# Kernel optimization log

Hardware: AMD Instinct MI355X
Metric: run time of the kernel (lower is better)

The kernel has to match this reference:

```python
import jax, jax.numpy as jnp
import numpy as np

RHO = 1.0          # ADMM penalty
LAM = 0.1          # lambda_sparse
MAX_ITERS = 20
ZETA = 0.05        # APAS drift threshold / CDS temperature
TAU = 0.1          # chiral stabilizer tolerance
STEP = 0.1         # gradient step size
COHESION = 1.0     # Mohr-Coulomb cohesion
MU = 0.5           # Mohr-Coulomb friction coefficient
DP_K = 10.0        # Drucker-Prager deviatoric-norm radius


def _pas(c):
    # Phase Alignment Invariant: scalar phase-coherence metric in [0,1]
    return jnp.abs(jnp.mean(jnp.cos(c)))


def _chirality(c):
    # odd (sign-sensitive) global moment
    return jnp.mean(c ** 3)


def _mc_proj(c, g):
    # Mohr-Coulomb yield projection: clamp magnitude to cohesion + mu*|grad|
    return jnp.sign(c) * jnp.minimum(jnp.abs(c), COHESION + MU * jnp.abs(g))


def _dp_proj(c):
    # Drucker-Prager: project deviatoric part onto norm ball of radius DP_K (per row)
    m = jnp.mean(c, axis=-1, keepdims=True)
    dev = c - m
    n = jnp.linalg.norm(dev, axis=-1, keepdims=True)
    scale = jnp.minimum(1.0, DP_K / (n + 1e-8))
    return m + dev * scale


def setup_inputs() -> dict:
    key = jax.random.key(0)
    k1, k2, k3 = jax.random.split(key, 3)
    B, D = 1024, 2048
    initial_c = 0.5 * jax.random.normal(k1, (B, D), dtype=jnp.float32)
    W = jax.random.normal(k2, (D, D), dtype=jnp.float32) / np.float32(np.sqrt(D))
    love_w = 1.0 + 0.01 * jax.random.normal(k3, (D,), dtype=jnp.float32)
    love_b = jnp.zeros((D,), dtype=jnp.float32)
    return {"initial_c": initial_c, "W": W, "love_w": love_w, "love_b": love_b}


def _forward(initial_c, W, love_w, love_b):
    c_sym = initial_c
    c0 = initial_c
    z0 = c0
    u0 = jnp.zeros_like(c0)
    prev_pas0 = _pas(c0)
    prev_score0 = -_chirality(c0)  # drift = 0 -> exp(0) = 1

    def step(carry, _):
        c, z, u, prev_pas, prev_score, low, done = carry

        def energy(ci):
            pred = ci @ W  # forward_op_fn
            violation_pressure = 0.5 * jnp.sum((pred - ci) ** 2)
            admm_tension = 0.5 * RHO * jnp.sum((ci - z + u) ** 2)
            return violation_pressure + admm_tension

        g = jax.grad(energy)(c)
        c_yield = _mc_proj(c, g)
        c_next = (c_yield * love_w + love_b) - STEP * g  # LoveVector then step
        z_in = c_next + u
        thr = LAM / RHO
        z_next = jnp.sign(z_in) * jnp.maximum(jnp.abs(z_in) - thr, 0.0)
        u_next = u + (c_next - z_next)

        cur_pas = _pas(c_next)
        drift = jnp.abs(cur_pas - prev_pas)
        violation = drift > ZETA
        low = jnp.where(cur_pas < 0.5, low + 1, 0)
        done = done | (low > 20)
        cur_score = -_chirality(c_next) * jnp.exp(-drift / ZETA)
        stable = (cur_score - prev_score) >= -TAU
        acc = (~violation) & stable & (~done)

        sel = lambda a, b: jnp.where(acc, a, b)
        new = (sel(c_next, c), sel(z_next, z), sel(u_next, u),
               jnp.where(acc, cur_pas, prev_pas),
               jnp.where(acc, cur_score, prev_score), low, done)
        return new, None

    init = (c0, z0, u0, prev_pas0, prev_score0,
            jnp.zeros((), jnp.int32), jnp.zeros((), jnp.bool_))
    (c_phys, z, u, _, _, _, _), _ = jax.lax.scan(step, init, None, length=MAX_ITERS)

    diff = jnp.linalg.norm(c_phys - c_sym)
    chi_cur = _chirality(c_phys)
    chi_orig = _chirality(c_sym)
    status = jnp.where(jnp.sign(chi_cur) != jnp.sign(chi_orig),
                       2,
                       jnp.where(diff > 5.0, 2, jnp.where(diff > 1.0, 1, 0))).astype(jnp.int32)

    delta = c_phys - c_sym
    symbolic_delta = jnp.round(delta * 10.0) / 10.0
    c_compressed = _dp_proj(c_sym + symbolic_delta)
    return c_compressed, status


def reference(initial_c, W, love_w, love_b):
    return _forward(initial_c, W, love_w, love_b)
```

## Files before the change

kernel.cpp:

```cpp
#include <hip/hip_runtime.h>
#include <math.h>

#define D 2048
#define BROWS 1024
#define NEL (D*BROWS)
#define NBLK 1024
#define NTHREADS_TOT (NBLK*256)

#define GM 64
#define GN 64
#define GK 16

__device__ __forceinline__ double blk_reduce(double v, double* sm) {
    const int t = threadIdx.x;
    sm[t] = v;
    __syncthreads();
    for (int s = 128; s > 0; s >>= 1) {
        if (t < s) sm[t] += sm[t + s];
        __syncthreads();
    }
    double r = sm[0];
    __syncthreads();
    return r;
}

__global__ __launch_bounds__(128, 2) void k_gemm(const float* __restrict__ A,
        const float* __restrict__ B, float* __restrict__ P0, float* __restrict__ P1,
        const float* __restrict__ Wadj, int ksz, int mode, const int* __restrict__ frz)
{
    if (frz && *frz) return;
    __shared__ float As[2][GK][GM + 4];
    __shared__ float Bs[2][GK][GN + 4];
    const int t  = threadIdx.x;
    const int tx = t & 7, ty = t >> 3;
    const int row0 = blockIdx.y * GM, col0 = blockIdx.x * GN;
    const int k0 = blockIdx.z * ksz;
    float* __restrict__ out = blockIdx.z ? P1 : P0;

    const int rs = t >> 2, qs = t & 3;
    const float* pA0 = A + (size_t)(row0 + rs) * D + (k0 + qs * 4);
    const float* pA1 = pA0 + (size_t)32 * D;
    const float* pB0 = B + (size_t)(col0 + rs) * D + (k0 + qs * 4);
    const float* pB1 = pB0 + (size_t)32 * D;

    float acc[4][8];
    #pragma unroll
    for (int i = 0; i < 4; ++i)
        #pragma unroll
        for (int j = 0; j < 8; ++j) acc[i][j] = 0.0f;

    const int ntiles = ksz / GK;
    float4 ga0, ga1, gb0, gb1;

#define LOADR { \
    ga0 = *reinterpret_cast<const float4*>(pA0); \
    ga1 = *reinterpret_cast<const float4*>(pA1); \
    gb0 = *reinterpret_cast<const float4*>(pB0); \
    gb1 = *reinterpret_cast<const float4*>(pB1); \
    pA0 += GK; pA1 += GK; pB0 += GK; pB1 += GK; }

#define STAGE(BUF) { \
    As[BUF][qs*4+0][rs] = ga0.x;  As[BUF][qs*4+1][rs] = ga0.y;  \
    As[BUF][qs*4+2][rs] = ga0.z;  As[BUF][qs*4+3][rs] = ga0.w;  \
    As[BUF][qs*4+0][rs+32] = ga1.x; As[BUF][qs*4+1][rs+32] = ga1.y; \
    As[BUF][qs*4+2][rs+32] = ga1.z; As[BUF][qs*4+3][rs+32] = ga1.w; \
    Bs[BUF][qs*4+0][rs] = gb0.x;  Bs[BUF][qs*4+1][rs] = gb0.y;  \
    Bs[BUF][qs*4+2][rs] = gb0.z;  Bs[BUF][qs*4+3][rs] = gb0.w;  \
    Bs[BUF][qs*4+0][rs+32] = gb1.x; Bs[BUF][qs*4+1][rs+32] = gb1.y; \
    Bs[BUF][qs*4+2][rs+32] = gb1.z; Bs[BUF][qs*4+3][rs+32] = gb1.w; }

#define COMPUTE(BUF) { \
    _Pragma("unroll") \
    for (int k = 0; k < GK; ++k) { \
        float a[4], b[8]; \
        *reinterpret_cast<float4*>(&a[0]) = *reinterpret_cast<const float4*>(&As[BUF][k][ty*4]); \
        *reinterpret_cast<float4*>(&b[0]) = *reinterpret_cast<const float4*>(&Bs[BUF][k][tx*4]); \
        *reinterpret_cast<float4*>(&b[4]) = *reinterpret_cast<const float4*>(&Bs[BUF][k][32 + tx*4]); \
        _Pragma("unroll") \
        for (int i = 0; i < 4; ++i) \
            _Pragma("unroll") \
            for (int j = 0; j < 8; ++j) \
                acc[i][j] += a[i] * b[j]; \
    } }

    LOADR;
    STAGE(0);
    __syncthreads();

    for (int tt = 0; tt < ntiles; tt += 2) {
        LOADR;
        COMPUTE(0);
        STAGE(1);
        __syncthreads();
        if (tt + 2 < ntiles) {
            LOADR;
            COMPUTE(1);
            STAGE(0);
            __syncthreads();
        } else {
            COMPUTE(1);
        }
    }

#undef LOADR
#undef STAGE
#undef COMPUTE

    #pragma unroll
    for (int i = 0; i < 4; ++i) {
        const int grow = row0 + ty*4 + i;
        float vv[8];
        #pragma unroll
        for (int j = 0; j < 8; ++j) vv[j] = acc[i][j];
        if (mode == 0) {
            #pragma unroll
            for (int j = 0; j < 8; ++j) {
                const int gcol = col0 + ((j < 4) ? (tx*4 + j) : (32 + tx*4 + j - 4));
                const float wsum = Wadj[(size_t)grow * D + gcol] + Wadj[(size_t)gcol * D + grow];
                vv[j] += (grow == gcol ? 1.0f : 0.0f) - wsum;
            }
        }
        float* orow = &out[(size_t)grow * D + col0];
        *reinterpret_cast<float4*>(&orow[tx*4]) =
            make_float4(vv[0], vv[1], vv[2], vv[3]);
        *reinterpret_cast<float4*>(&orow[32 + tx*4]) =
            make_float4(vv[4], vv[5], vv[6], vv[7]);
    }
}

__global__ __launch_bounds__(256) void k_init(const float* __restrict__ c0,
        float* __restrict__ c, float* __restrict__ z, float* __restrict__ u,
        double* __restrict__ partials)
{
    __shared__ double sm[256];
    double sc = 0.0, s3 = 0.0;
    const int tid = blockIdx.x * 256 + threadIdx.x;
    const float4 zero4 = make_float4(0.f, 0.f, 0.f, 0.f);
    for (int i4 = tid; i4 < NEL/4; i4 += NTHREADS_TOT) {
        const float4 v4 = reinterpret_cast<const float4*>(c0)[i4];
        reinterpret_cast<float4*>(c)[i4] = v4;
        reinterpret_cast<float4*>(z)[i4] = v4;
        reinterpret_cast<float4*>(u)[i4] = zero4;
        const float va[4] = {v4.x, v4.y, v4.z, v4.w};
        #pragma unroll
        for (int L = 0; L < 4; ++L) {
            sc += (double)cosf(va[L]);
            s3 += (double)((va[L] * va[L]) * va[L]);
        }
    }
    const double tc = blk_reduce(sc, sm);
    const double t3 = blk_reduce(s3, sm);
    if (threadIdx.x == 0) { partials[blockIdx.x] = tc; partials[NBLK + blockIdx.x] = t3; }
}

__global__ __launch_bounds__(256) void k_decide0(const double* __restrict__ partials,
        double* __restrict__ scal, int* __restrict__ flag, int* __restrict__ frz,
        int* __restrict__ sel)
{
    __shared__ double sm[256];
    const int t = threadIdx.x;
    const double a = partials[t] + partials[t+256] + partials[t+512] + partials[t+768];
    const double b = partials[NBLK+t] + partials[NBLK+t+256] + partials[NBLK+t+512] + partials[NBLK+t+768];
    const double tc = blk_reduce(a, sm);
    const double t3 = blk_reduce(b, sm);
    if (t == 0) {
        const double pas = fabs(tc / (double)NEL);
        const double chi = t3 / (double)NEL;
        scal[0] = pas; scal[1] = -chi; scal[2] = chi;
        *flag = 0; *frz = 0; *sel = 0;
    }
}

__global__ __launch_bounds__(256) void k_elem_pp(const float* __restrict__ P0,
        const float* __restrict__ P1, const float* __restrict__ cc,
        float* __restrict__ cn, float* __restrict__ z, float* __restrict__ u,
        const float* __restrict__ lw, const float* __restrict__ lb,
        double* __restrict__ partials, const int* __restrict__ frz)
{
#pragma clang fp contract(off)
    if (*frz) return;
    __shared__ double sm[256];
    double sc = 0.0, s3 = 0.0;
    const int tid = blockIdx.x * 256 + threadIdx.x;
    for (int i4 = tid; i4 < NEL/4; i4 += NTHREADS_TOT) {
        const int j4 = i4 & (D/4 - 1);
        const float4 p0 = reinterpret_cast<const float4*>(P0)[i4];
        const float4 p1 = reinterpret_cast<const float4*>(P1)[i4];
        const float4 cv4 = reinterpret_cast<const float4*>(cc)[i4];
        const float4 zv4 = reinterpret_cast<const float4*>(z)[i4];
        const float4 uv4 = reinterpret_cast<const float4*>(u)[i4];
        const float4 w4 = reinterpret_cast<const float4*>(lw)[j4];
        const float4 b4 = reinterpret_cast<const float4*>(lb)[j4];
        const float p0a[4] = {p0.x, p0.y, p0.z, p0.w};
        const float p1a[4] = {p1.x, p1.y, p1.z, p1.w};
        const float cva[4] = {cv4.x, cv4.y, cv4.z, cv4.w};
        const float zva[4] = {zv4.x, zv4.y, zv4.z, zv4.w};
        const float uva[4] = {uv4.x, uv4.y, uv4.z, uv4.w};
        const float w4a[4] = {w4.x, w4.y, w4.z, w4.w};
        const float b4a[4] = {b4.x, b4.y, b4.z, b4.w};
        float Rc[4], Rz[4], Ru[4];
        #pragma unroll
        for (int L = 0; L < 4; ++L) {
            const float cv = cva[L];
            const float uv = uva[L];
            const float g = (p0a[L] + p1a[L]) + ((cv - zva[L]) + uv);
            const float lim = 1.0f + 0.5f * fabsf(g);
            const float mn = fminf(fabsf(cv), lim);
            const float cy = (cv > 0.0f) ? mn : ((cv < 0.0f) ? -mn : 0.0f);
            const float cnv = (cy * w4a[L] + b4a[L]) - 0.1f * g;
            Rc[L] = cnv;
            const float zi = cnv + uv;
            float zm = fabsf(zi) - 0.1f;
            zm = fmaxf(zm, 0.0f);
            const float zn = (zi > 0.0f) ? zm : ((zi < 0.0f) ? -zm : 0.0f);
            Rz[L] = zn;
            Ru[L] = uv + (cnv - zn);
            sc += (double)cosf(cnv);
            s3 += (double)((cnv * cnv) * cnv);
        }
        reinterpret_cast<float4*>(cn)[i4] = make_float4(Rc[0], Rc[1], Rc[2], Rc[3]);
        reinterpret_cast<float4*>(z)[i4]  = make_float4(Rz[0], Rz[1], Rz[2], Rz[3]);
        reinterpret_cast<float4*>(u)[i4]  = make_float4(Ru[0], Ru[1], Ru[2], Ru[3]);
    }
    const double tc = blk_reduce(sc, sm);
    const double t3 = blk_reduce(s3, sm);
    if (threadIdx.x == 0) { partials[blockIdx.x] = tc; partials[NBLK + blockIdx.x] = t3; }
}

__global__ __launch_bounds__(256) void k_elem(float* __restrict__ P0,
        const float* __restrict__ P1, const float* __restrict__ c,
        const float* __restrict__ z, const float* __restrict__ u,
        const float* __restrict__ lw, const float* __restrict__ lb,
        double* __restrict__ partials, const int* __restrict__ frz)
{
#pragma clang fp contract(off)
    if (*frz) return;
    __shared__ double sm[256];
    double sc = 0.0, s3 = 0.0;
    const int tid = blockIdx.x * 256 + threadIdx.x;
    for (int i = tid; i < NEL; i += NTHREADS_TOT) {
        const int j = i & (D - 1);
        const float cv = c[i];
        const float g = (P0[i] + P1[i]) + ((cv - z[i]) + u[i]);
        const float lim = 1.0f + 0.5f * fabsf(g);
        const float mn = fminf(fabsf(cv), lim);
        const float cy = (cv > 0.0f) ? mn : ((cv < 0.0f) ? -mn : 0.0f);
        const float cnv = (cy * lw[j] + lb[j]) - 0.1f * g;
        P0[i] = cnv;
        sc += (double)cosf(cnv);
        s3 += (double)((cnv * cnv) * cnv);
    }
    const double tc = blk_reduce(sc, sm);
    const double t3 = blk_reduce(s3, sm);
    if (threadIdx.x == 0) { partials[blockIdx.x] = tc; partials[NBLK + blockIdx.x] = t3; }
}

__global__ __launch_bounds__(256) void k_decide(const double* __restrict__ partials,
        double* __restrict__ scal, int* __restrict__ flag, int* __restrict__ frz,
        int* __restrict__ sel, int next_sel)
{
    __shared__ double sm[256];
    if (*frz) return;
    const int t = threadIdx.x;
    const double a = partials[t] + partials[t+256] + partials[t+512] + partials[t+768];
    const double b = partials[NBLK+t] + partials[NBLK+t+256] + partials[NBLK+t+512] + partials[NBLK+t+768];
    const double tc = blk_reduce(a, sm);
    const double t3 = blk_reduce(b, sm);
    if (t == 0) {
        const double pas = fabs(tc / (double)NEL);
        const double drift = fabs(pas - scal[0]);
        const double chi = t3 / (double)NEL;
        const double score = -chi * exp(-drift / 0.05);
        const bool violation = drift > 0.05;
        const bool stable = (score - scal[1]) >= -0.1;
        const int acc = (!violation && stable) ? 1 : 0;
        *flag = acc;
        if (acc) { scal[0] = pas; scal[1] = score; *sel = next_sel; }
        else     { *frz = 1; }
    }
}

__global__ __launch_bounds__(256) void k_commit(const float* __restrict__ cn,
        float* __restrict__ c, float* __restrict__ z, float* __restrict__ u,
        const int* __restrict__ flag)
{
#pragma clang fp contract(off)
    if (*flag == 0) return;
    const int tid = blockIdx.x * 256 + threadIdx.x;
    for (int i = tid; i < NEL; i += NTHREADS_TOT) {
        const float cnv = cn[i];
        const float uv = u[i];
        const float zi = cnv + uv;
        float zm = fabsf(zi) - 0.1f;
        zm = fmaxf(zm, 0.0f);
        const float zn = (zi > 0.0f) ? zm : ((zi < 0.0f) ? -zm : 0.0f);
        c[i] = cnv;
        z[i] = zn;
        u[i] = uv + (cnv - zn);
    }
}

__global__ __launch_bounds__(256) void k_final_rows(const float* __restrict__ c0,
        const float* __restrict__ cA, const float* __restrict__ cB,
        const int* __restrict__ sel, float* __restrict__ outp)
{
#pragma clang fp contract(off)
    __shared__ double sm[256];
    const float* __restrict__ c = (*sel) ? cB : cA;
    const int row = blockIdx.x;
    const size_t base = (size_t)row * D;
    float tv[8];
    double s1 = 0.0;
    #pragma unroll
    for (int s = 0; s < 8; ++s) {
        const int j = threadIdx.x + s * 256;
        const float s0 = c0[base + j];
        const float delta = c[base + j] - s0;
        const float sym = rintf(delta * 10.0f) / 10.0f;
        const float tval = s0 + sym;
        tv[s] = tval;
        s1 += (double)tval;
    }
    const double tot = blk_reduce(s1, sm);
    const float m = (float)(tot / (double)D);
    double s2 = 0.0;
    #pragma unroll
    for (int s = 0; s < 8; ++s) {
        const float dev = tv[s] - m;
        s2 += (double)(dev * dev);
    }
    const double tot2 = blk_reduce(s2, sm);
    const float n = sqrtf((float)tot2);
    const float scale = fminf(1.0f, 10.0f / (n + 1e-8f));
    #pragma unroll
    for (int s = 0; s < 8; ++s) {
        const int j = threadIdx.x + s * 256;
        outp[base + j] = m + (tv[s] - m) * scale;
    }
}

__global__ __launch_bounds__(256) void k_final_glob(const float* __restrict__ c0,
        const float* __restrict__ cA, const float* __restrict__ cB,
        const int* __restrict__ sel, double* __restrict__ partials)
{
    __shared__ double sm[256];
    const float* __restrict__ c = (*sel) ? cB : cA;
    double s3 = 0.0, sd = 0.0;
    const int tid = blockIdx.x * 256 + threadIdx.x;
    for (int i = tid; i < NEL; i += NTHREADS_TOT) {
        const float v = c[i];
        s3 += (double)((v * v) * v);
        const float d = v - c0[i];
        sd += (double)(d * d);
    }
    const double t3 = blk_reduce(s3, sm);
    const double td = blk_reduce(sd, sm);
    if (threadIdx.x == 0) { partials[blockIdx.x] = t3; partials[NBLK + blockIdx.x] = td; }
}

__global__ __launch_bounds__(256) void k_final_status(const double* __restrict__ partials,
        const double* __restrict__ scal, float* __restrict__ outp)
{
    __shared__ double sm[256];
    const int t = threadIdx.x;
    const double a = partials[t] + partials[t+256] + partials[t+512] + partials[t+768];
    const double b = partials[NBLK+t] + partials[NBLK+t+256] + partials[NBLK+t+512] + partials[NBLK+t+768];
    const double t3 = blk_reduce(a, sm);
    const double td = blk_reduce(b, sm);
    if (t == 0) {
        const double chi_cur = t3 / (double)NEL;
        const double diff = sqrt(td);
        const double chi_orig = scal[2];
        const int s_cur = (chi_cur > 0.0) - (chi_cur < 0.0);
        const int s_org = (chi_orig > 0.0) - (chi_orig < 0.0);
        int status;
        if (s_cur != s_org)   status = 2;
        else if (diff > 5.0)  status = 2;
        else if (diff > 1.0)  status = 1;
        else                  status = 0;
        outp[NEL] = (float)status;
    }
}

extern "C" void kernel_launch(void* const* d_in, const int* in_sizes, int n_in,
                              void* d_out, int out_size, void* d_ws, size_t ws_size,
                              hipStream_t stream)
{
    const float* c0 = (const float*)d_in[0];
    const float* W  = (const float*)d_in[1];
    const float* lw = (const float*)d_in[2];
    const float* lb = (const float*)d_in[3];
    float* outp = (float*)d_out;

    const size_t M4 = (size_t)D * D;
    const size_t N4 = (size_t)NEL;
    float* Mb = (float*)d_ws;
    float* region = Mb + M4;

    const size_t tail_bytes = (2 * NBLK + 8) * sizeof(double) + 4 * sizeof(int);
    const bool pp = ws_size >= (M4 + 6 * N4) * sizeof(float) + tail_bytes;

    float *cA, *cB, *z, *u, *P0, *P1;
    if (pp) { cA = region; cB = cA + N4; z = cB + N4; u = z + N4; P0 = u + N4; P1 = P0 + N4; }
    else    { cA = region; cB = cA;      z = cA + N4; u = z + N4; P0 = u + N4; P1 = P0 + N4; }
    double* partials = (double*)(P1 + N4);
    double* scal = partials + 2 * NBLK;
    int* flag = (int*)(scal + 8);
    int* frz  = flag + 1;
    int* sel  = frz + 1;

    k_gemm<<<dim3(D / GN, D / GM, 1), 128, 0, stream>>>(W, W, Mb, Mb, W, D, 0, nullptr);
    k_init<<<NBLK, 256, 0, stream>>>(c0, cA, z, u, partials);
    k_decide0<<<1, 256, 0, stream>>>(partials, scal, flag, frz, sel);

    for (int t = 0; t < 20; ++t) {
        const float* ccur = (pp && (t & 1)) ? cB : cA;
        float* cnxt = (pp && !(t & 1)) ? cB : cA;
        k_gemm<<<dim3(D / GN, BROWS / GM, 2), 128, 0, stream>>>(ccur, Mb, P0, P1, nullptr, D / 2, 1, frz);
        if (pp) {
            k_elem_pp<<<NBLK, 256, 0, stream>>>(P0, P1, ccur, cnxt, z, u, lw, lb, partials, frz);
            k_decide<<<1, 256, 0, stream>>>(partials, scal, flag, frz, sel, (t + 1) & 1);
        } else {
            k_elem<<<NBLK, 256, 0, stream>>>(P0, P1, cA, z, u, lw, lb, partials, frz);
            k_decide<<<1, 256, 0, stream>>>(partials, scal, flag, frz, sel, 0);
            k_commit<<<NBLK, 256, 0, stream>>>(P0, cA, z, u, flag);
        }
    }

    k_final_rows<<<BROWS, 256, 0, stream>>>(c0, cA, cB, sel, outp);
    k_final_glob<<<NBLK, 256, 0, stream>>>(c0, cA, cB, sel, partials);
    k_final_status<<<1, 256, 0, stream>>>(partials, scal, outp);
}
```

Baseline: 2.927 ms.

## Use single-wavefront GEMM blocks with 8x8 per-thread tiles, drop barriers

The fp32 GEMM block shrinks from 128 to 64 threads, so each thread now accumulates an 8x8 output micro-tile instead of 4x8. Each thread loads four float4 rows of A and B per K-tile. With the block being a single wavefront, the __syncthreads barriers around the double-buffered LDS staging are removed. The aim is more FMA reuse per LDS read and less barrier overhead, at the cost of more registers and fewer resident waves per CU. It also relies on in-order wavefront execution for LDS correctness.

```diff
diff --git a/kernel.cpp b/kernel.cpp
--- a/kernel.cpp
+++ b/kernel.cpp
@@ -24,7 +24,7 @@
     return r;
 }
 
-__global__ __launch_bounds__(128, 2) void k_gemm(const float* __restrict__ A,
+__global__ __launch_bounds__(64, 2) void k_gemm(const float* __restrict__ A,
         const float* __restrict__ B, float* __restrict__ P0, float* __restrict__ P1,
         const float* __restrict__ Wadj, int ksz, int mode, const int* __restrict__ frz)
 {
@@ -38,46 +38,58 @@
     float* __restrict__ out = blockIdx.z ? P1 : P0;
 
     const int rs = t >> 2, qs = t & 3;
-    const float* pA0 = A + (size_t)(row0 + rs) * D + (k0 + qs * 4);
-    const float* pA1 = pA0 + (size_t)32 * D;
-    const float* pB0 = B + (size_t)(col0 + rs) * D + (k0 + qs * 4);
-    const float* pB1 = pB0 + (size_t)32 * D;
-
-    float acc[4][8];
+    const float* pA = A + (size_t)(row0 + rs) * D + (k0 + qs * 4);
+    const float* pB = B + (size_t)(col0 + rs) * D + (k0 + qs * 4);
+    const size_t R16 = (size_t)16 * D, R32 = (size_t)32 * D, R48 = (size_t)48 * D;
+
+    float acc[8][8];
     #pragma unroll
-    for (int i = 0; i < 4; ++i)
+    for (int i = 0; i < 8; ++i)
         #pragma unroll
         for (int j = 0; j < 8; ++j) acc[i][j] = 0.0f;
 
     const int ntiles = ksz / GK;
-    float4 ga0, ga1, gb0, gb1;
+    float4 ra0, ra1, ra2, ra3, rb0, rb1, rb2, rb3;
 
 #define LOADR { \
-    ga0 = *reinterpret_cast<const float4*>(pA0); \
-    ga1 = *reinterpret_cast<const float4*>(pA1); \
-    gb0 = *reinterpret_cast<const float4*>(pB0); \
-    gb1 = *reinterpret_cast<const float4*>(pB1); \
-    pA0 += GK; pA1 += GK; pB0 += GK; pB1 += GK; }
+    ra0 = *reinterpret_cast<const float4*>(pA);       \
+    ra1 = *reinterpret_cast<const float4*>(pA + R16); \
+    ra2 = *reinterpret_cast<const float4*>(pA + R32); \
+    ra3 = *reinterpret_cast<const float4*>(pA + R48); \
+    rb0 = *reinterpret_cast<const float4*>(pB);       \
+    rb1 = *reinterpret_cast<const float4*>(pB + R16); \
+    rb2 = *reinterpret_cast<const float4*>(pB + R32); \
+    rb3 = *reinterpret_cast<const float4*>(pB + R48); \
+    pA += GK; pB += GK; }
 
 #define STAGE(BUF) { \
-    As[BUF][qs*4+0][rs] = ga0.x;  As[BUF][qs*4+1][rs] = ga0.y;  \
-    As[BUF][qs*4+2][rs] = ga0.z;  As[BUF][qs*4+3][rs] = ga0.w;  \
-    As[BUF][qs*4+0][rs+32] = ga1.x; As[BUF][qs*4+1][rs+32] = ga1.y; \
-    As[BUF][qs*4+2][rs+32] = ga1.z; As[BUF][qs*4+3][rs+32] = ga1.w; \
-    Bs[BUF][qs*4+0][rs] = gb0.x;  Bs[BUF][qs*4+1][rs] = gb0.y;  \
-    Bs[BUF][qs*4+2][rs] = gb0.z;  Bs[BUF][qs*4+3][rs] = gb0.w;  \
-    Bs[BUF][qs*4+0][rs+32] = gb1.x; Bs[BUF][qs*4+1][rs+32] = gb1.y; \
-    Bs[BUF][qs*4+2][rs+32] = gb1.z; Bs[BUF][qs*4+3][rs+32] = gb1.w; }
+    As[BUF][qs*4+0][rs] = ra0.x;    As[BUF][qs*4+1][rs] = ra0.y;    \
+    As[BUF][qs*4+2][rs] = ra0.z;    As[BUF][qs*4+3][rs] = ra0.w;    \
+    As[BUF][qs*4+0][rs+16] = ra1.x; As[BUF][qs*4+1][rs+16] = ra1.y; \
+    As[BUF][qs*4+2][rs+16] = ra1.z; As[BUF][qs*4+3][rs+16] = ra1.w; \
+    As[BUF][qs*4+0][rs+32] = ra2.x; As[BUF][qs*4+1][rs+32] = ra2.y; \
+    As[BUF][qs*4+2][rs+32] = ra2.z; As[BUF][qs*4+3][rs+32] = ra2.w; \
+    As[BUF][qs*4+0][rs+48] = ra3.x; As[BUF][qs*4+1][rs+48] = ra3.y; \
+    As[BUF][qs*4+2][rs+48] = ra3.z; As[BUF][qs*4+3][rs+48] = ra3.w; \
+    Bs[BUF][qs*4+0][rs] = rb0.x;    Bs[BUF][qs*4+1][rs] = rb0.y;    \
+    Bs[BUF][qs*4+2][rs] = rb0.z;    Bs[BUF][qs*4+3][rs] = rb0.w;    \
+    Bs[BUF][qs*4+0][rs+16] = rb1.x; Bs[BUF][qs*4+1][rs+16] = rb1.y; \
+    Bs[BUF][qs*4+2][rs+16] = rb1.z; Bs[BUF][qs*4+3][rs+16] = rb1.w; \
+    Bs[BUF][qs*4+0][rs+32] = rb2.x; Bs[BUF][qs*4+1][rs+32] = rb2.y; \
+    Bs[BUF][qs*4+2][rs+32] = rb2.z; Bs[BUF][qs*4+3][rs+32] = rb2.w; \
+    Bs[BUF][qs*4+0][rs+48] = rb3.x; Bs[BUF][qs*4+1][rs+48] = rb3.y; \
+    Bs[BUF][qs*4+2][rs+48] = rb3.z; Bs[BUF][qs*4+3][rs+48] = rb3.w; }
 
 #define COMPUTE(BUF) { \
     _Pragma("unroll") \
     for (int k = 0; k < GK; ++k) { \
-        float a[4], b[8]; \
+        float a[8], b[8]; \
         *reinterpret_cast<float4*>(&a[0]) = *reinterpret_cast<const float4*>(&As[BUF][k][ty*4]); \
+        *reinterpret_cast<float4*>(&a[4]) = *reinterpret_cast<const float4*>(&As[BUF][k][32 + ty*4]); \
         *reinterpret_cast<float4*>(&b[0]) = *reinterpret_cast<const float4*>(&Bs[BUF][k][tx*4]); \
         *reinterpret_cast<float4*>(&b[4]) = *reinterpret_cast<const float4*>(&Bs[BUF][k][32 + tx*4]); \
         _Pragma("unroll") \
-        for (int i = 0; i < 4; ++i) \
+        for (int i = 0; i < 8; ++i) \
             _Pragma("unroll") \
             for (int j = 0; j < 8; ++j) \
                 acc[i][j] += a[i] * b[j]; \
@@ -85,18 +97,15 @@
 
     LOADR;
     STAGE(0);
-    __syncthreads();
 
     for (int tt = 0; tt < ntiles; tt += 2) {
         LOADR;
         COMPUTE(0);
         STAGE(1);
-        __syncthreads();
         if (tt + 2 < ntiles) {
             LOADR;
             COMPUTE(1);
             STAGE(0);
-            __syncthreads();
         } else {
             COMPUTE(1);
         }
@@ -107,8 +116,8 @@
 #undef COMPUTE
 
     #pragma unroll
-    for (int i = 0; i < 4; ++i) {
-        const int grow = row0 + ty*4 + i;
+    for (int i = 0; i < 8; ++i) {
+        const int grow = row0 + ((i < 4) ? (ty*4 + i) : (32 + ty*4 + i - 4));
         float vv[8];
         #pragma unroll
         for (int j = 0; j < 8; ++j) vv[j] = acc[i][j];
@@ -409,14 +418,14 @@
     int* frz  = flag + 1;
     int* sel  = frz + 1;
 
-    k_gemm<<<dim3(D / GN, D / GM, 1), 128, 0, stream>>>(W, W, Mb, Mb, W, D, 0, nullptr);
+    k_gemm<<<dim3(D / GN, D / GM, 1), 64, 0, stream>>>(W, W, Mb, Mb, W, D, 0, nullptr);
     k_init<<<NBLK, 256, 0, stream>>>(c0, cA, z, u, partials);
     k_decide0<<<1, 256, 0, stream>>>(partials, scal, flag, frz, sel);
 
     for (int t = 0; t < 20; ++t) {
         const float* ccur = (pp && (t & 1)) ? cB : cA;
         float* cnxt = (pp && !(t & 1)) ? cB : cA;
-        k_gemm<<<dim3(D / GN, BROWS / GM, 2), 128, 0, stream>>>(ccur, Mb, P0, P1, nullptr, D / 2, 1, frz);
+        k_gemm<<<dim3(D / GN, BROWS / GM, 2), 64, 0, stream>>>(ccur, Mb, P0, P1, nullptr, D / 2, 1, frz);
         if (pp) {
             k_elem_pp<<<NBLK, 256, 0, stream>>>(P0, P1, ccur, cnxt, z, u, lw, lb, partials, frz);
             k_decide<<<1, 256, 0, stream>>>(partials, scal, flag, frz, sel, (t + 1) & 1);
```

Result: slower. 4.888 ms (+67.0%).
